# Kernel optimization log

Hardware: AMD Instinct MI355X
Metric: run time of the kernel (lower is better)

The kernel has to match this reference:

```python
import jax, jax.numpy as jnp
import numpy as np

N = 50000   # nodes
E = 600000  # edges (avg degree ~12)
R = 8       # num_relations = 2 * n_speakers**2, n_speakers=2
B = 32      # num_bases = args.batch_size
GD, H1, H2 = 128, 128, 128


def setup_inputs() -> dict:
    key = jax.random.key(0)
    ks = jax.random.split(key, 16)
    w = lambda k, shape: jax.random.normal(k, shape, jnp.float32) * 0.05
    return {
        "node_features": jax.random.normal(ks[0], (N, GD), jnp.float32),
        "edge_index": jax.random.randint(ks[1], (2, E), 0, N),
        "edge_norm": jax.random.uniform(ks[2], (E,), jnp.float32),
        "edge_type": jax.random.randint(ks[3], (E,), 0, R),
        "basis": w(ks[4], (B, GD, H1)),
        "comp": w(ks[5], (R, B)),
        "root": w(ks[6], (GD, H1)),
        "bias1": jnp.zeros((H1,), jnp.float32),
        "w_key": w(ks[7], (H1, H2)),
        "b_key": jnp.zeros((H2,), jnp.float32),
        "w_query": w(ks[8], (H1, H2)),
        "b_query": jnp.zeros((H2,), jnp.float32),
        "w_value": w(ks[9], (H1, H2)),
        "b_value": jnp.zeros((H2,), jnp.float32),
        "w_skip": w(ks[10], (H1, H2)),
        "b_skip": jnp.zeros((H2,), jnp.float32),
    }


def reference(node_features, edge_index, edge_norm, edge_type, basis, comp,
              root, bias1, w_key, b_key, w_query, b_query, w_value, b_value,
              w_skip, b_skip):
    n = node_features.shape[0]
    r = comp.shape[0]
    src, dst = edge_index[0], edge_index[1]

    # ---- RGCNConv (basis decomposition, per-relation mean aggregation) ----
    W = jnp.einsum('rb,bio->rio', comp, basis)            # [R, GD, H1]
    xW = jnp.einsum('ni,rio->rno', node_features, W)      # [R, N, H1]
    msg = xW[edge_type, src]                              # [E, H1]
    seg = edge_type * n + dst                             # combined (relation, dst) segment id
    agg = jax.ops.segment_sum(msg, seg, num_segments=r * n).reshape(r, n, -1)
    cnt = jax.ops.segment_sum(jnp.ones(msg.shape[0], jnp.float32), seg,
                              num_segments=r * n).reshape(r, n, 1)
    h = (agg / jnp.maximum(cnt, 1.0)).sum(0) + node_features @ root + bias1

    # ---- ResGatedGraphConv: sigmoid(k_i + q_j) * v_j, sum-aggregated + skip ----
    k = h @ w_key + b_key
    q = h @ w_query + b_query
    v = h @ w_value + b_value
    m = jax.nn.sigmoid(k[dst] + q[src]) * v[src]          # [E, H2]
    out = jax.ops.segment_sum(m, dst, num_segments=n) + h @ w_skip + b_skip
    return out
```

## Files before the change

### kernel.cpp

```cpp
#include <hip/hip_runtime.h>
#include <stdint.h>

#define GD 128
#define H1 128
#define H2 128
#define NBASES 32
#define NREL 8
#define K1 (NREL*GD + GD)

typedef __attribute__((ext_vector_type(8))) short bf16x8;
typedef __attribute__((ext_vector_type(4))) float f32x4;

static inline size_t align256(size_t x){ return (x + 255) & ~(size_t)255; }

__device__ __forceinline__ float bf2f(uint32_t u16){
  union { uint32_t u; float f; } c; c.u = (u16 & 0xffffu) << 16; return c.f;
}
__device__ __forceinline__ unsigned short f2bf(float f){
  union { float f; uint32_t u; } c; c.f = f;
  uint32_t u = c.u;
  u += 0x7fffu + ((u >> 16) & 1u);
  return (unsigned short)(u >> 16);
}
__device__ __forceinline__ uint32_t pkbf(float a, float b){
  union { float f; uint32_t u; } ca, cb; ca.f = a; cb.f = b;
  return __builtin_amdgcn_perm(cb.u + 0x8000u, ca.u + 0x8000u, 0x07060302u);
}

__device__ __forceinline__ void async_copy16(void* lds_dst, const void* gsrc){
  __builtin_amdgcn_global_load_lds(
      (const __attribute__((address_space(1))) uint32_t*)gsrc,
      (__attribute__((address_space(3))) uint32_t*)lds_dst, 16, 0, 0);
}

__global__ void k_build_B1t(const float* __restrict__ comp, const float* __restrict__ basis,
                            const float* __restrict__ root, unsigned short* __restrict__ B1t){
  int idx = blockIdx.x*blockDim.x + threadIdx.x;
  if (idx >= H1*K1) return;
  int nn = idx / K1, kk = idx % K1;
  float v;
  if (kk < NREL*GD){
    int r = kk >> 7, i = kk & 127;
    float acc = 0.f;
    #pragma unroll
    for (int b = 0; b < NBASES; ++b)
      acc += comp[r*NBASES + b] * basis[((size_t)b*GD + i)*H1 + nn];
    v = acc;
  } else {
    v = root[(size_t)(kk - NREL*GD)*H1 + nn];
  }
  B1t[idx] = f2bf(v);
}

__global__ void k_build_B2t(const float* __restrict__ wk, const float* __restrict__ wq,
                            const float* __restrict__ wv, const float* __restrict__ wsk,
                            const float* __restrict__ bk, const float* __restrict__ bq,
                            const float* __restrict__ bv, const float* __restrict__ bs,
                            unsigned short* __restrict__ B2t, float* __restrict__ Bb){
  int idx = blockIdx.x*blockDim.x + threadIdx.x;
  if (idx < 512*H1){
    int c = idx / H1, k = idx % H1;
    const float* w = (c < 128) ? wk : (c < 256) ? wq : (c < 384) ? wv : wsk;
    B2t[idx] = f2bf(w[(size_t)k*H2 + (c & 127)]);
  }
  if (idx < 512){
    const float* b = (idx < 128) ? bk : (idx < 256) ? bq : (idx < 384) ? bv : bs;
    Bb[idx] = b[idx & 127];
  }
}

__global__ void k_cast_x4(const float4* __restrict__ x, uint2* __restrict__ xout, int cnt4){
  int i = blockIdx.x*blockDim.x + threadIdx.x;
  if (i >= cnt4) return;
  float4 v = x[i];
  uint2 o; o.x = pkbf(v.x, v.y); o.y = pkbf(v.z, v.w);
  xout[i] = o;
}

__global__ void k_hist_rd(const int* __restrict__ dst, const int* __restrict__ typ,
                          int* __restrict__ cnt, int E, int n){
  int e = blockIdx.x*blockDim.x + threadIdx.x;
  if (e < E) atomicAdd(&cnt[typ[e]*n + dst[e]], 1);
}

__global__ void k_scanA(const int* __restrict__ deg, int* __restrict__ off,
                        int* __restrict__ btot, int len){
  __shared__ int wsum[16];
  int t = threadIdx.x, lane = t & 63, w = t >> 6;
  int i0 = blockIdx.x*8192 + t*8;
  int v[8];
  if (i0 + 7 < len){
    int4 va = *(const int4*)(deg + i0);
    int4 vb = *(const int4*)(deg + i0 + 4);
    v[0]=va.x; v[1]=va.y; v[2]=va.z; v[3]=va.w;
    v[4]=vb.x; v[5]=vb.y; v[6]=vb.z; v[7]=vb.w;
  } else {
    #pragma unroll
    for (int u = 0; u < 8; ++u) v[u] = (i0+u < len) ? deg[i0+u] : 0;
  }
  int s[8]; s[0] = v[0];
  #pragma unroll
  for (int u = 1; u < 8; ++u) s[u] = s[u-1] + v[u];
  int x = s[7];
  #pragma unroll
  for (int d = 1; d < 64; d <<= 1){
    int u = __shfl_up(x, d, 64);
    if (lane >= d) x += u;
  }
  if (lane == 63) wsum[w] = x;
  __syncthreads();
  if (t < 16){
    int y = wsum[t];
    #pragma unroll
    for (int d = 1; d < 16; d <<= 1){
      int u = __shfl_up(y, d, 16);
      if (t >= d) y += u;
    }
    wsum[t] = y;
  }
  __syncthreads();
  int woff = (w > 0) ? wsum[w-1] : 0;
  int excl = woff + x - s[7];
  #pragma unroll
  for (int u = 0; u < 8; ++u)
    if (i0+u < len) off[i0+u] = excl + s[u] - v[u];
  if (t == 0) btot[blockIdx.x] = wsum[15];
}

__global__ void k_scanB(const int* __restrict__ btot, int* __restrict__ off,
                        int* __restrict__ cursor, int len, int sentinel){
  int t = threadIdx.x, bid = blockIdx.x;
  int add = 0;
  for (int j = 0; j < bid; ++j) add += btot[j];
  int i0 = bid*8192 + t*8;
  #pragma unroll
  for (int u = 0; u < 8; ++u){
    int i = i0 + u;
    if (i < len){ int val = off[i] + add; off[i] = val; cursor[i] = val; }
  }
  if (bid == 0 && t == 0) off[len] = sentinel;
}

__global__ void k_scatter_rd(const int* __restrict__ src, const int* __restrict__ dst,
                             const int* __restrict__ typ, int* __restrict__ cursor,
                             int* __restrict__ pk, int E, int n){
  int e = blockIdx.x*blockDim.x + threadIdx.x;
  if (e >= E) return;
  int pos = atomicAdd(&cursor[typ[e]*n + dst[e]], 1);
  pk[pos] = src[e];
}

__global__ void k_edge1(const int* __restrict__ off_rd, const int* __restrict__ pk_rd,
                        const unsigned short* __restrict__ xbf,
                        unsigned short* __restrict__ Abig, int n, int npad){
  int wid = blockIdx.x*(blockDim.x >> 6) + (threadIdx.x >> 6);
  int lane = threadIdx.x & 63;
  if (wid >= npad) return;
  uint32_t* Arow = (uint32_t*)(Abig + (size_t)wid*K1);
  if (wid >= n){
    #pragma unroll
    for (int r = 0; r < 9; ++r) Arow[r*64 + lane] = 0u;
    return;
  }
  const uint32_t* x32 = (const uint32_t*)xbf;
  int r8 = lane & 7;
  int o_r = off_rd[(size_t)r8*n + wid];
  int e_r = off_rd[(size_t)r8*n + wid + 1];
  int c_r = e_r - o_r;
  int c0_ = __builtin_amdgcn_readlane(c_r, 0), c1_ = __builtin_amdgcn_readlane(c_r, 1);
  int c2_ = __builtin_amdgcn_readlane(c_r, 2), c3_ = __builtin_amdgcn_readlane(c_r, 3);
  int c4_ = __builtin_amdgcn_readlane(c_r, 4), c5_ = __builtin_amdgcn_readlane(c_r, 5);
  int c6_ = __builtin_amdgcn_readlane(c_r, 6), c7_ = __builtin_amdgcn_readlane(c_r, 7);
  int o0_ = __builtin_amdgcn_readlane(o_r, 0), o1_ = __builtin_amdgcn_readlane(o_r, 1);
  int o2_ = __builtin_amdgcn_readlane(o_r, 2), o3_ = __builtin_amdgcn_readlane(o_r, 3);
  int o4_ = __builtin_amdgcn_readlane(o_r, 4), o5_ = __builtin_amdgcn_readlane(o_r, 5);
  int o6_ = __builtin_amdgcn_readlane(o_r, 6), o7_ = __builtin_amdgcn_readlane(o_r, 7);
  int p1 = c0_, p2 = p1 + c1_, p3 = p2 + c2_, p4 = p3 + c3_;
  int p5 = p4 + c4_, p6 = p5 + c5_, p7 = p6 + c6_, dg = p7 + c7_;

  float a0[8], a1[8];
  #pragma unroll
  for (int r = 0; r < 8; ++r){ a0[r] = 0.f; a1[r] = 0.f; }

  for (int jb = 0; jb < dg; jb += 64){
    int i = jb + lane;
    int adj = o0_, rel = 0;
    adj = (i >= p1) ? (o1_ - p1) : adj;  rel += (i >= p1);
    adj = (i >= p2) ? (o2_ - p2) : adj;  rel += (i >= p2);
    adj = (i >= p3) ? (o3_ - p3) : adj;  rel += (i >= p3);
    adj = (i >= p4) ? (o4_ - p4) : adj;  rel += (i >= p4);
    adj = (i >= p5) ? (o5_ - p5) : adj;  rel += (i >= p5);
    adj = (i >= p6) ? (o6_ - p6) : adj;  rel += (i >= p6);
    adj = (i >= p7) ? (o7_ - p7) : adj;  rel += (i >= p7);
    int m = dg - jb; if (m > 64) m = 64;
    int pj = (lane < m) ? pk_rd[adj + i] : 0;
    int jj = 0;
    for (; jj + 8 <= m; jj += 8){
      uint32_t g[8]; int rr[8];
      #pragma unroll
      for (int k = 0; k < 8; ++k){
        int s = __builtin_amdgcn_readlane(pj, jj + k);
        rr[k] = __builtin_amdgcn_readlane(rel, jj + k);
        g[k] = x32[(size_t)s*64 + lane];
      }
      #pragma unroll
      for (int k = 0; k < 8; ++k){
        float x0 = bf2f(g[k]), x1 = bf2f(g[k] >> 16);
        switch (rr[k]){
          case 0: a0[0]+=x0; a1[0]+=x1; break;
          case 1: a0[1]+=x0; a1[1]+=x1; break;
          case 2: a0[2]+=x0; a1[2]+=x1; break;
          case 3: a0[3]+=x0; a1[3]+=x1; break;
          case 4: a0[4]+=x0; a1[4]+=x1; break;
          case 5: a0[5]+=x0; a1[5]+=x1; break;
          case 6: a0[6]+=x0; a1[6]+=x1; break;
          default: a0[7]+=x0; a1[7]+=x1; break;
        }
      }
    }
    for (; jj < m; ++jj){
      int s = __builtin_amdgcn_readlane(pj, jj);
      int rk = __builtin_amdgcn_readlane(rel, jj);
      uint32_t gg = x32[(size_t)s*64 + lane];
      float x0 = bf2f(gg), x1 = bf2f(gg >> 16);
      switch (rk){
        case 0: a0[0]+=x0; a1[0]+=x1; break;
        case 1: a0[1]+=x0; a1[1]+=x1; break;
        case 2: a0[2]+=x0; a1[2]+=x1; break;
        case 3: a0[3]+=x0; a1[3]+=x1; break;
        case 4: a0[4]+=x0; a1[4]+=x1; break;
        case 5: a0[5]+=x0; a1[5]+=x1; break;
        case 6: a0[6]+=x0; a1[6]+=x1; break;
        default: a0[7]+=x0; a1[7]+=x1; break;
      }
    }
  }
  int cc[8] = {c0_, c1_, c2_, c3_, c4_, c5_, c6_, c7_};
  #pragma unroll
  for (int r = 0; r < 8; ++r){
    float inv = (cc[r] > 0) ? 1.f/(float)cc[r] : 0.f;
    Arow[r*64 + lane] = pkbf(a0[r]*inv, a1[r]*inv);
  }
  Arow[512 + lane] = x32[(size_t)wid*64 + lane];
}

__launch_bounds__(256)
__global__ void k_gemm1(const unsigned short* __restrict__ A, const unsigned short* __restrict__ Bt,
                        const float* __restrict__ bias, unsigned short* __restrict__ h){
  __shared__ char lds[16384];
  int t = threadIdx.x, lane = t & 63, wave = t >> 6;
  int row0 = blockIdx.x * 128;
  int mrow = lane & 15, quad = lane >> 4;
  int wrow = (wave & 1) * 64, wcol = (wave >> 1) * 64;
  int s = (mrow >> 1) & 3;

  const unsigned short* Asrc = A + (size_t)(row0 + (t >> 2))*K1 + (((t & 3) ^ ((t >> 3) & 3)) << 3);
  const unsigned short* Bsrc = Bt + (size_t)(t >> 2)*K1 + (((t & 3) ^ ((t >> 3) & 3)) << 3);
  char* ldsw = lds + wave*1024;

  int aoff = (wrow + mrow)*64 + ((quad ^ s) << 4);
  int boff = 8192 + (wcol + mrow)*64 + ((quad ^ s) << 4);

  f32x4 acc[4][4];
  #pragma unroll
  for (int i = 0; i < 4; ++i)
    #pragma unroll
    for (int j = 0; j < 4; ++j) acc[i][j] = (f32x4){0.f,0.f,0.f,0.f};

  for (int kt = 0; kt < K1; kt += 32){
    __syncthreads();
    async_copy16(ldsw,         Asrc + kt);
    async_copy16(ldsw + 4096,  Asrc + (size_t)64*K1 + kt);
    async_copy16(ldsw + 8192,  Bsrc + kt);
    async_copy16(ldsw + 12288, Bsrc + (size_t)64*K1 + kt);
    __syncthreads();
    bf16x8 af[4], bf[4];
    #pragma unroll
    for (int i = 0; i < 4; ++i) af[i] = *(const bf16x8*)(lds + aoff + i*1024);
    #pragma unroll
    for (int j = 0; j < 4; ++j) bf[j] = *(const bf16x8*)(lds + boff + j*1024);
    #pragma unroll
    for (int i = 0; i < 4; ++i)
      #pragma unroll
      for (int j = 0; j < 4; ++j)
        acc[i][j] = __builtin_amdgcn_mfma_f32_16x16x32_bf16(af[i], bf[j], acc[i][j], 0, 0, 0);
  }
  #pragma unroll
  for (int j = 0; j < 4; ++j){
    int col = wcol + j*16 + mrow;
    float bcol = bias[col];
    #pragma unroll
    for (int i = 0; i < 4; ++i)
      #pragma unroll
      for (int rg = 0; rg < 4; ++rg){
        int row = wrow + i*16 + quad*4 + rg;
        h[(size_t)(row0 + row)*H1 + col] = f2bf(acc[i][j][rg] + bcol);
      }
  }
}

__launch_bounds__(256)
__global__ void k_gemm2(const unsigned short* __restrict__ A, const unsigned short* __restrict__ Bt,
                        const float* __restrict__ Bb, unsigned short* __restrict__ kqv,
                        float* __restrict__ out, int n){
  __shared__ char lds[16384];
  int t = threadIdx.x, lane = t & 63, wave = t >> 6;
  int row0 = blockIdx.x * 128;
  int c0 = blockIdx.y * 128;
  int mrow = lane & 15, quad = lane >> 4;
  int wrow = (wave & 1) * 64, wcol = (wave >> 1) * 64;
  int s = (mrow >> 1) & 3;

  const unsigned short* Asrc = A + (size_t)(row0 + (t >> 2))*H1 + (((t & 3) ^ ((t >> 3) & 3)) << 3);
  const unsigned short* Bsrc = Bt + (size_t)(c0 + (t >> 2))*H1 + (((t & 3) ^ ((t >> 3) & 3)) << 3);
  char* ldsw = lds + wave*1024;

  int aoff = (wrow + mrow)*64 + ((quad ^ s) << 4);
  int boff = 8192 + (wcol + mrow)*64 + ((quad ^ s) << 4);

  f32x4 acc[4][4];
  #pragma unroll
  for (int i = 0; i < 4; ++i)
    #pragma unroll
    for (int j = 0; j < 4; ++j) acc[i][j] = (f32x4){0.f,0.f,0.f,0.f};

  #pragma unroll
  for (int kt = 0; kt < H1; kt += 32){
    __syncthreads();
    async_copy16(ldsw,         Asrc + kt);
    async_copy16(ldsw + 4096,  Asrc + (size_t)64*H1 + kt);
    async_copy16(ldsw + 8192,  Bsrc + kt);
    async_copy16(ldsw + 12288, Bsrc + (size_t)64*H1 + kt);
    __syncthreads();
    bf16x8 af[4], bf[4];
    #pragma unroll
    for (int i = 0; i < 4; ++i) af[i] = *(const bf16x8*)(lds + aoff + i*1024);
    #pragma unroll
    for (int j = 0; j < 4; ++j) bf[j] = *(const bf16x8*)(lds + boff + j*1024);
    #pragma unroll
    for (int i = 0; i < 4; ++i)
      #pragma unroll
      for (int j = 0; j < 4; ++j)
        acc[i][j] = __builtin_amdgcn_mfma_f32_16x16x32_bf16(af[i], bf[j], acc[i][j], 0, 0, 0);
  }
  #pragma unroll
  for (int j = 0; j < 4; ++j){
    int col = c0 + wcol + j*16 + mrow;
    float bcol = Bb[col];
    #pragma unroll
    for (int i = 0; i < 4; ++i)
      #pragma unroll
      for (int rg = 0; rg < 4; ++rg){
        int rr = row0 + wrow + i*16 + quad*4 + rg;
        if (rr >= n) continue;
        float v = acc[i][j][rg] + bcol;
        if (col < 128){
          kqv[(size_t)rr*384 + col] = f2bf(v);
        } else if (col < 256){
          int jj = col - 128;
          kqv[(size_t)rr*384 + 128 + ((jj >> 1) << 2) + (jj & 1)] = f2bf(v);
        } else if (col < 384){
          int jj = col - 256;
          kqv[(size_t)rr*384 + 128 + ((jj >> 1) << 2) + 2 + (jj & 1)] = f2bf(v);
        } else {
          out[(size_t)rr*H2 + (col - 384)] = v;
        }
      }
  }
}

__global__ void k_edge2(const int* __restrict__ off_rd, const int* __restrict__ pk_rd,
                        const unsigned short* __restrict__ kqv, float* __restrict__ out, int n){
  int wid = blockIdx.x*(blockDim.x >> 6) + (threadIdx.x >> 6);
  int lane = threadIdx.x & 63;
  if (wid >= n) return;
  const uint32_t* kv32 = (const uint32_t*)kqv;
  int r = lane & 7;
  int o_r = off_rd[(size_t)r*n + wid];
  int e_r = off_rd[(size_t)r*n + wid + 1];
  int c_r = e_r - o_r;
  int c0_ = __builtin_amdgcn_readlane(c_r, 0), c1_ = __builtin_amdgcn_readlane(c_r, 1);
  int c2_ = __builtin_amdgcn_readlane(c_r, 2), c3_ = __builtin_amdgcn_readlane(c_r, 3);
  int c4_ = __builtin_amdgcn_readlane(c_r, 4), c5_ = __builtin_amdgcn_readlane(c_r, 5);
  int c6_ = __builtin_amdgcn_readlane(c_r, 6), c7_ = __builtin_amdgcn_readlane(c_r, 7);
  int o0_ = __builtin_amdgcn_readlane(o_r, 0), o1_ = __builtin_amdgcn_readlane(o_r, 1);
  int o2_ = __builtin_amdgcn_readlane(o_r, 2), o3_ = __builtin_amdgcn_readlane(o_r, 3);
  int o4_ = __builtin_amdgcn_readlane(o_r, 4), o5_ = __builtin_amdgcn_readlane(o_r, 5);
  int o6_ = __builtin_amdgcn_readlane(o_r, 6), o7_ = __builtin_amdgcn_readlane(o_r, 7);
  int p1 = c0_, p2 = p1 + c1_, p3 = p2 + c2_, p4 = p3 + c3_;
  int p5 = p4 + c4_, p6 = p5 + c5_, p7 = p6 + c6_, dg = p7 + c7_;

  uint32_t ku = kv32[(size_t)wid*192 + lane];
  float k0 = bf2f(ku), k1 = bf2f(ku >> 16);
  float a0 = 0.f, a1 = 0.f;
  for (int jb = 0; jb < dg; jb += 64){
    int i = jb + lane;
    int adj = o0_;
    adj = (i >= p1) ? (o1_ - p1) : adj;
    adj = (i >= p2) ? (o2_ - p2) : adj;
    adj = (i >= p3) ? (o3_ - p3) : adj;
    adj = (i >= p4) ? (o4_ - p4) : adj;
    adj = (i >= p5) ? (o5_ - p5) : adj;
    adj = (i >= p6) ? (o6_ - p6) : adj;
    adj = (i >= p7) ? (o7_ - p7) : adj;
    int m = dg - jb; if (m > 64) m = 64;
    int pj = (lane < m) ? pk_rd[adj + i] : 0;
    int jj = 0;
    for (; jj + 4 <= m; jj += 4){
      int s0 = __builtin_amdgcn_readlane(pj, jj);
      int s1 = __builtin_amdgcn_readlane(pj, jj+1);
      int s2 = __builtin_amdgcn_readlane(pj, jj+2);
      int s3 = __builtin_amdgcn_readlane(pj, jj+3);
      uint2 q0 = *(const uint2*)(kv32 + (size_t)s0*192 + 64 + lane*2);
      uint2 q1 = *(const uint2*)(kv32 + (size_t)s1*192 + 64 + lane*2);
      uint2 q2 = *(const uint2*)(kv32 + (size_t)s2*192 + 64 + lane*2);
      uint2 q3 = *(const uint2*)(kv32 + (size_t)s3*192 + 64 + lane*2);
      #pragma unroll
      for (int k = 0; k < 4; ++k){
        uint2 qc = (k==0)?q0:(k==1)?q1:(k==2)?q2:q3;
        float qq0 = bf2f(qc.x), qq1 = bf2f(qc.x >> 16);
        float vv0 = bf2f(qc.y), vv1 = bf2f(qc.y >> 16);
        float g0 = 1.f / (1.f + __expf(-(k0 + qq0)));
        float g1 = 1.f / (1.f + __expf(-(k1 + qq1)));
        a0 += g0*vv0; a1 += g1*vv1;
      }
    }
    for (; jj < m; ++jj){
      int s0 = __builtin_amdgcn_readlane(pj, jj);
      uint2 qc = *(const uint2*)(kv32 + (size_t)s0*192 + 64 + lane*2);
      float qq0 = bf2f(qc.x), qq1 = bf2f(qc.x >> 16);
      float vv0 = bf2f(qc.y), vv1 = bf2f(qc.y >> 16);
      float g0 = 1.f / (1.f + __expf(-(k0 + qq0)));
      float g1 = 1.f / (1.f + __expf(-(k1 + qq1)));
      a0 += g0*vv0; a1 += g1*vv1;
    }
  }
  float2* op = (float2*)(out + (size_t)wid*H2);
  float2 cur = op[lane];
  cur.x += a0; cur.y += a1;
  op[lane] = cur;
}

extern "C" void kernel_launch(void* const* d_in, const int* in_sizes, int n_in,
                              void* d_out, int out_size, void* d_ws, size_t ws_size,
                              hipStream_t stream){
  const float* x     = (const float*)d_in[0];
  const int*   eidx  = (const int*)  d_in[1];
  const int*   etype = (const int*)  d_in[3];
  const float* basis = (const float*)d_in[4];
  const float* comp  = (const float*)d_in[5];
  const float* root  = (const float*)d_in[6];
  const float* bias1 = (const float*)d_in[7];
  const float* wk    = (const float*)d_in[8];
  const float* bk    = (const float*)d_in[9];
  const float* wq    = (const float*)d_in[10];
  const float* bq    = (const float*)d_in[11];
  const float* wv    = (const float*)d_in[12];
  const float* bv    = (const float*)d_in[13];
  const float* wsk   = (const float*)d_in[14];
  const float* bs    = (const float*)d_in[15];
  const int n = in_sizes[0] / GD;
  const int E = in_sizes[3];
  const int npad = (n + 127) & ~127;
  const int* esrc = eidx;
  const int* edst = eidx + E;
  float* out = (float*)d_out;

  char* w = (char*)d_ws;
  size_t off = 0;
  unsigned short* xbf  = (unsigned short*)(w + off); off = align256(off + (size_t)n*GD*2);
  unsigned short* Abig = (unsigned short*)(w + off); off = align256(off + (size_t)npad*K1*2);
  unsigned short* B1t  = (unsigned short*)(w + off); off = align256(off + (size_t)H1*K1*2);
  unsigned short* B2t  = (unsigned short*)(w + off); off = align256(off + (size_t)512*H1*2);
  float* Bb            = (float*)(w + off);          off = align256(off + 512*4);
  unsigned short* hbuf = (unsigned short*)(w + off); off = align256(off + (size_t)npad*H1*2);
  unsigned short* kqv  = (unsigned short*)(w + off); off = align256(off + (size_t)n*384*2);
  int* cnt_rd          = (int*)(w + off);            off = align256(off + (size_t)(8*n+1)*4);
  int* off_rd          = (int*)(w + off);            off = align256(off + (size_t)(8*n+1)*4);
  int* cur_rd          = (int*)(w + off);            off = align256(off + (size_t)8*n*4);
  int* btot_rd         = (int*)(w + off);            off = align256(off + 64*4);
  int* pk_rd           = (int*)(w + off);            off = align256(off + (size_t)E*4);

  const int nblk_rd = (8*n + 8191) / 8192;

  hipMemsetAsync(cnt_rd, 0, (size_t)8*n*4, stream);

  k_build_B1t<<<(H1*K1 + 255)/256, 256, 0, stream>>>(comp, basis, root, B1t);
  k_build_B2t<<<(512*H1 + 255)/256, 256, 0, stream>>>(wk, wq, wv, wsk, bk, bq, bv, bs, B2t, Bb);
  k_cast_x4<<<((n*GD/4) + 255)/256, 256, 0, stream>>>((const float4*)x, (uint2*)xbf, n*GD/4);
  k_hist_rd<<<(E + 255)/256, 256, 0, stream>>>(edst, etype, cnt_rd, E, n);
  k_scanA<<<nblk_rd, 1024, 0, stream>>>(cnt_rd, off_rd, btot_rd, 8*n);
  k_scanB<<<nblk_rd, 1024, 0, stream>>>(btot_rd, off_rd, cur_rd, 8*n, E);
  k_scatter_rd<<<(E + 255)/256, 256, 0, stream>>>(esrc, edst, etype, cur_rd, pk_rd, E, n);
  k_edge1<<<(npad + 3)/4, 256, 0, stream>>>(off_rd, pk_rd, xbf, Abig, n, npad);
  k_gemm1<<<npad/128, 256, 0, stream>>>(Abig, B1t, bias1, hbuf);
  k_gemm2<<<dim3(npad/128, 4), 256, 0, stream>>>(hbuf, B2t, Bb, kqv, out, n);
  k_edge2<<<(n + 3)/4, 256, 0, stream>>>(off_rd, pk_rd, kqv, out, n);
}
```

Before: 396.8 us.

## Fuse prep kernels, stream Abig stores, store skip in bf16, deepen edge2 unroll

Merges the B1t/B2t weight builds, the x-to-bf16 cast and the count-array zeroing into a single k_prep launch, which removes three launches and a memset. Abig stores in edge1 become nontemporal to avoid polluting cache. The skip projection is written as a bf16 buffer and added in edge2, replacing an fp32 read-modify-write of the output; this adds bf16 rounding to the skip term. The edge2 gather loop is unrolled from 4 to 8 to keep more loads in flight.

```diff
diff --git a/kernel.cpp b/kernel.cpp
--- a/kernel.cpp
+++ b/kernel.cpp
@@ -33,48 +33,55 @@
       (__attribute__((address_space(3))) uint32_t*)lds_dst, 16, 0, 0);
 }
 
-__global__ void k_build_B1t(const float* __restrict__ comp, const float* __restrict__ basis,
-                            const float* __restrict__ root, unsigned short* __restrict__ B1t){
-  int idx = blockIdx.x*blockDim.x + threadIdx.x;
-  if (idx >= H1*K1) return;
-  int nn = idx / K1, kk = idx % K1;
-  float v;
-  if (kk < NREL*GD){
-    int r = kk >> 7, i = kk & 127;
-    float acc = 0.f;
-    #pragma unroll
-    for (int b = 0; b < NBASES; ++b)
-      acc += comp[r*NBASES + b] * basis[((size_t)b*GD + i)*H1 + nn];
-    v = acc;
-  } else {
-    v = root[(size_t)(kk - NREL*GD)*H1 + nn];
-  }
-  B1t[idx] = f2bf(v);
-}
-
-__global__ void k_build_B2t(const float* __restrict__ wk, const float* __restrict__ wq,
-                            const float* __restrict__ wv, const float* __restrict__ wsk,
-                            const float* __restrict__ bk, const float* __restrict__ bq,
-                            const float* __restrict__ bv, const float* __restrict__ bs,
-                            unsigned short* __restrict__ B2t, float* __restrict__ Bb){
-  int idx = blockIdx.x*blockDim.x + threadIdx.x;
-  if (idx < 512*H1){
+__global__ void k_prep(const float* __restrict__ comp, const float* __restrict__ basis,
+                       const float* __restrict__ root, unsigned short* __restrict__ B1t,
+                       const float* __restrict__ wk, const float* __restrict__ wq,
+                       const float* __restrict__ wv, const float* __restrict__ wsk,
+                       const float* __restrict__ bk, const float* __restrict__ bq,
+                       const float* __restrict__ bv, const float* __restrict__ bs,
+                       unsigned short* __restrict__ B2t, float* __restrict__ Bb,
+                       const float4* __restrict__ x, uint2* __restrict__ xout, int cnt4,
+                       int4* __restrict__ cntz, int nz4){
+  int b = blockIdx.x, t = threadIdx.x;
+  if (b < 576){
+    int idx = b*256 + t;
+    int nn = idx / K1, kk = idx % K1;
+    float v;
+    if (kk < NREL*GD){
+      int r = kk >> 7, i = kk & 127;
+      float acc = 0.f;
+      #pragma unroll
+      for (int bb = 0; bb < NBASES; ++bb)
+        acc += comp[r*NBASES + bb] * basis[((size_t)bb*GD + i)*H1 + nn];
+      v = acc;
+    } else {
+      v = root[(size_t)(kk - NREL*GD)*H1 + nn];
+    }
+    B1t[idx] = f2bf(v);
+  } else if (b < 576 + 256){
+    int idx = (b - 576)*256 + t;
     int c = idx / H1, k = idx % H1;
     const float* w = (c < 128) ? wk : (c < 256) ? wq : (c < 384) ? wv : wsk;
     B2t[idx] = f2bf(w[(size_t)k*H2 + (c & 127)]);
-  }
-  if (idx < 512){
-    const float* b = (idx < 128) ? bk : (idx < 256) ? bq : (idx < 384) ? bv : bs;
-    Bb[idx] = b[idx & 127];
-  }
-}
-
-__global__ void k_cast_x4(const float4* __restrict__ x, uint2* __restrict__ xout, int cnt4){
-  int i = blockIdx.x*blockDim.x + threadIdx.x;
-  if (i >= cnt4) return;
-  float4 v = x[i];
-  uint2 o; o.x = pkbf(v.x, v.y); o.y = pkbf(v.z, v.w);
-  xout[i] = o;
+    if (idx < 512){
+      const float* bia = (idx < 128) ? bk : (idx < 256) ? bq : (idx < 384) ? bv : bs;
+      Bb[idx] = bia[idx & 127];
+    }
+  } else {
+    int cb = b - (576 + 256);
+    int ncastb = (cnt4 + 255) >> 8;
+    if (cb < ncastb){
+      int i = cb*256 + t;
+      if (i < cnt4){
+        float4 v = x[i];
+        uint2 o; o.x = pkbf(v.x, v.y); o.y = pkbf(v.z, v.w);
+        xout[i] = o;
+      }
+    } else {
+      int i = (cb - ncastb)*256 + t;
+      if (i < nz4) cntz[i] = (int4){0,0,0,0};
+    }
+  }
 }
 
 __global__ void k_hist_rd(const int* __restrict__ dst, const int* __restrict__ typ,
@@ -159,7 +166,7 @@
   uint32_t* Arow = (uint32_t*)(Abig + (size_t)wid*K1);
   if (wid >= n){
     #pragma unroll
-    for (int r = 0; r < 9; ++r) Arow[r*64 + lane] = 0u;
+    for (int r = 0; r < 9; ++r) __builtin_nontemporal_store(0u, Arow + r*64 + lane);
     return;
   }
   const uint32_t* x32 = (const uint32_t*)xbf;
@@ -239,9 +246,9 @@
   #pragma unroll
   for (int r = 0; r < 8; ++r){
     float inv = (cc[r] > 0) ? 1.f/(float)cc[r] : 0.f;
-    Arow[r*64 + lane] = pkbf(a0[r]*inv, a1[r]*inv);
-  }
-  Arow[512 + lane] = x32[(size_t)wid*64 + lane];
+    __builtin_nontemporal_store(pkbf(a0[r]*inv, a1[r]*inv), Arow + r*64 + lane);
+  }
+  __builtin_nontemporal_store(x32[(size_t)wid*64 + lane], Arow + 512 + lane);
 }
 
 __launch_bounds__(256)
@@ -302,7 +309,7 @@
 __launch_bounds__(256)
 __global__ void k_gemm2(const unsigned short* __restrict__ A, const unsigned short* __restrict__ Bt,
                         const float* __restrict__ Bb, unsigned short* __restrict__ kqv,
-                        float* __restrict__ out, int n){
+                        unsigned short* __restrict__ skipb, int n){
   __shared__ char lds[16384];
   int t = threadIdx.x, lane = t & 63, wave = t >> 6;
   int row0 = blockIdx.x * 128;
@@ -363,14 +370,16 @@
           int jj = col - 256;
           kqv[(size_t)rr*384 + 128 + ((jj >> 1) << 2) + 2 + (jj & 1)] = f2bf(v);
         } else {
-          out[(size_t)rr*H2 + (col - 384)] = v;
+          skipb[(size_t)rr*H2 + (col - 384)] = f2bf(v);
         }
       }
   }
 }
 
 __global__ void k_edge2(const int* __restrict__ off_rd, const int* __restrict__ pk_rd,
-                        const unsigned short* __restrict__ kqv, float* __restrict__ out, int n){
+                        const unsigned short* __restrict__ kqv,
+                        const unsigned short* __restrict__ skipb,
+                        float* __restrict__ out, int n){
   int wid = blockIdx.x*(blockDim.x >> 6) + (threadIdx.x >> 6);
   int lane = threadIdx.x & 63;
   if (wid >= n) return;
@@ -406,28 +415,25 @@
     int m = dg - jb; if (m > 64) m = 64;
     int pj = (lane < m) ? pk_rd[adj + i] : 0;
     int jj = 0;
-    for (; jj + 4 <= m; jj += 4){
-      int s0 = __builtin_amdgcn_readlane(pj, jj);
-      int s1 = __builtin_amdgcn_readlane(pj, jj+1);
-      int s2 = __builtin_amdgcn_readlane(pj, jj+2);
-      int s3 = __builtin_amdgcn_readlane(pj, jj+3);
-      uint2 q0 = *(const uint2*)(kv32 + (size_t)s0*192 + 64 + lane*2);
-      uint2 q1 = *(const uint2*)(kv32 + (size_t)s1*192 + 64 + lane*2);
-      uint2 q2 = *(const uint2*)(kv32 + (size_t)s2*192 + 64 + lane*2);
-      uint2 q3 = *(const uint2*)(kv32 + (size_t)s3*192 + 64 + lane*2);
-      #pragma unroll
-      for (int k = 0; k < 4; ++k){
-        uint2 qc = (k==0)?q0:(k==1)?q1:(k==2)?q2:q3;
-        float qq0 = bf2f(qc.x), qq1 = bf2f(qc.x >> 16);
-        float vv0 = bf2f(qc.y), vv1 = bf2f(qc.y >> 16);
+    for (; jj + 8 <= m; jj += 8){
+      uint2 q[8];
+      #pragma unroll
+      for (int k = 0; k < 8; ++k){
+        int s = __builtin_amdgcn_readlane(pj, jj + k);
+        q[k] = *(const uint2*)(kv32 + (size_t)s*192 + 64 + lane*2);
+      }
+      #pragma unroll
+      for (int k = 0; k < 8; ++k){
+        float qq0 = bf2f(q[k].x), qq1 = bf2f(q[k].x >> 16);
+        float vv0 = bf2f(q[k].y), vv1 = bf2f(q[k].y >> 16);
         float g0 = 1.f / (1.f + __expf(-(k0 + qq0)));
         float g1 = 1.f / (1.f + __expf(-(k1 + qq1)));
         a0 += g0*vv0; a1 += g1*vv1;
       }
     }
     for (; jj < m; ++jj){
-      int s0 = __builtin_amdgcn_readlane(pj, jj);
-      uint2 qc = *(const uint2*)(kv32 + (size_t)s0*192 + 64 + lane*2);
+      int s = __builtin_amdgcn_readlane(pj, jj);
+      uint2 qc = *(const uint2*)(kv32 + (size_t)s*192 + 64 + lane*2);
       float qq0 = bf2f(qc.x), qq1 = bf2f(qc.x >> 16);
       float vv0 = bf2f(qc.y), vv1 = bf2f(qc.y >> 16);
       float g0 = 1.f / (1.f + __expf(-(k0 + qq0)));
@@ -435,10 +441,9 @@
       a0 += g0*vv0; a1 += g1*vv1;
     }
   }
-  float2* op = (float2*)(out + (size_t)wid*H2);
-  float2 cur = op[lane];
-  cur.x += a0; cur.y += a1;
-  op[lane] = cur;
+  uint32_t sk = ((const uint32_t*)skipb)[(size_t)wid*64 + lane];
+  float2 cur; cur.x = a0 + bf2f(sk); cur.y = a1 + bf2f(sk >> 16);
+  ((float2*)(out + (size_t)wid*H2))[lane] = cur;
 }
 
 extern "C" void kernel_launch(void* const* d_in, const int* in_sizes, int n_in,
@@ -475,25 +480,28 @@
   float* Bb            = (float*)(w + off);          off = align256(off + 512*4);
   unsigned short* hbuf = (unsigned short*)(w + off); off = align256(off + (size_t)npad*H1*2);
   unsigned short* kqv  = (unsigned short*)(w + off); off = align256(off + (size_t)n*384*2);
-  int* cnt_rd          = (int*)(w + off);            off = align256(off + (size_t)(8*n+1)*4);
+  unsigned short* skipb= (unsigned short*)(w + off); off = align256(off + (size_t)npad*H2*2);
+  int* cnt_rd          = (int*)(w + off);            off = align256(off + (size_t)(8*n+4)*4);
   int* off_rd          = (int*)(w + off);            off = align256(off + (size_t)(8*n+1)*4);
   int* cur_rd          = (int*)(w + off);            off = align256(off + (size_t)8*n*4);
   int* btot_rd         = (int*)(w + off);            off = align256(off + 64*4);
   int* pk_rd           = (int*)(w + off);            off = align256(off + (size_t)E*4);
 
   const int nblk_rd = (8*n + 8191) / 8192;
-
-  hipMemsetAsync(cnt_rd, 0, (size_t)8*n*4, stream);
-
-  k_build_B1t<<<(H1*K1 + 255)/256, 256, 0, stream>>>(comp, basis, root, B1t);
-  k_build_B2t<<<(512*H1 + 255)/256, 256, 0, stream>>>(wk, wq, wv, wsk, bk, bq, bv, bs, B2t, Bb);
-  k_cast_x4<<<((n*GD/4) + 255)/256, 256, 0, stream>>>((const float4*)x, (uint2*)xbf, n*GD/4);
+  const int cnt4 = n*GD/4;
+  const int nz4  = (8*n + 3)/4;
+  const int ncastb = (cnt4 + 255)/256;
+  const int nzerob = (nz4 + 255)/256;
+
+  k_prep<<<576 + 256 + ncastb + nzerob, 256, 0, stream>>>(
+      comp, basis, root, B1t, wk, wq, wv, wsk, bk, bq, bv, bs, B2t, Bb,
+      (const float4*)x, (uint2*)xbf, cnt4, (int4*)cnt_rd, nz4);
   k_hist_rd<<<(E + 255)/256, 256, 0, stream>>>(edst, etype, cnt_rd, E, n);
   k_scanA<<<nblk_rd, 1024, 0, stream>>>(cnt_rd, off_rd, btot_rd, 8*n);
   k_scanB<<<nblk_rd, 1024, 0, stream>>>(btot_rd, off_rd, cur_rd, 8*n, E);
   k_scatter_rd<<<(E + 255)/256, 256, 0, stream>>>(esrc, edst, etype, cur_rd, pk_rd, E, n);
   k_edge1<<<(npad + 3)/4, 256, 0, stream>>>(off_rd, pk_rd, xbf, Abig, n, npad);
   k_gemm1<<<npad/128, 256, 0, stream>>>(Abig, B1t, bias1, hbuf);
-  k_gemm2<<<dim3(npad/128, 4), 256, 0, stream>>>(hbuf, B2t, Bb, kqv, out, n);
-  k_edge2<<<(n + 3)/4, 256, 0, stream>>>(off_rd, pk_rd, kqv, out, n);
-}
+  k_gemm2<<<dim3(npad/128, 4), 256, 0, stream>>>(hbuf, B2t, Bb, kqv, skipb, n);
+  k_edge2<<<(n + 3)/4, 256, 0, stream>>>(off_rd, pk_rd, kqv, skipb, out, n);
+}
```

New measurement: 390.8 us. About the same (-1.5%).
